# Kernel optimization log

Hardware: AMD Instinct MI355X
Metric: run time of the kernel (lower is better)

The kernel has to match this reference:

```python
import jax, jax.numpy as jnp
import numpy as np


def setup_inputs() -> dict:
    key = jax.random.key(0)
    k1, k2 = jax.random.split(key)
    x = jax.random.normal(k1, (64, 32, 32, 128), dtype=jnp.float32)
    embeddings = jax.random.normal(k2, (128, 1024), dtype=jnp.float32)  # (embedding_dim, num_embeddings)
    return {"x": x, "embeddings": embeddings}


def reference(x, embeddings):
    d = embeddings.shape[0]
    flat = x.reshape(-1, d)  # [N, d]
    # squared L2 distances: ||f||^2 + ||e||^2 - 2 f.e
    similarity = flat @ embeddings  # [N, K]
    distances = (jnp.sum(flat * flat, axis=1, keepdims=True)
                 + jnp.sum(embeddings * embeddings, axis=0)
                 - 2.0 * similarity)
    idx = jnp.argmin(distances, axis=1)  # [N]
    # gather codes (equivalent to one_hot @ embeddings^T)
    quantized = embeddings.T[idx].reshape(x.shape)
    # straight-through estimator
    quantized = x + jax.lax.stop_gradient(quantized - x)
    return quantized
```

## Files before the change

kernel.cpp:

```cpp
#include <hip/hip_runtime.h>


#define NROWS 65536
#define DDIM 128
#define KCODES 1024
#define MARGIN1 0.30f

typedef __attribute__((ext_vector_type(8))) short short8;
typedef __attribute__((ext_vector_type(16))) float f32x16;

__device__ inline ushort f2bf(float f) {
    union { float f; unsigned u; } v; v.f = f;
    unsigned r = v.u + 0x7fffu + ((v.u >> 16) & 1u);
    return (ushort)(r >> 16);
}
__device__ inline float bf2f(ushort b) {
    union { unsigned u; float f; } v; v.u = ((unsigned)b) << 16;
    return v.f;
}

__device__ inline void gload_lds16(const uint4* g, uint4* lds) {
    __builtin_amdgcn_global_load_lds((const __attribute__((address_space(1))) void*)g,
                                     (__attribute__((address_space(3))) void*)lds,
                                     16, 0, 0);
}

__global__ void k_prep(const float* __restrict__ x, const float* __restrict__ e,
                       float* __restrict__ et, float* __restrict__ nrm,
                       double* __restrict__ nrm64, uint4* __restrict__ epq,
                       unsigned* __restrict__ nhl, uint4* __restrict__ xp,
                       int* __restrict__ wlc) {
    const int gid = blockIdx.x * blockDim.x + threadIdx.x;

    if (gid == 0) { wlc[0] = 0; wlc[1] = 0; }

    {
        int lane = gid & 63, c = (gid >> 6) & 7, rt = gid >> 9;
        int row = rt * 32 + (lane & 31);
        int kbase = c * 16 + ((lane >> 5) << 3);
        const float4* xr4 = reinterpret_cast<const float4*>(x + (size_t)row * DDIM + kbase);
        float4 u = xr4[0], v = xr4[1];
        float fv[8] = {u.x, u.y, u.z, u.w, v.x, v.y, v.z, v.w};
        union { ushort s[8]; uint4 q; } pk;
        #pragma unroll
        for (int j = 0; j < 8; ++j) pk.s[j] = f2bf(fv[j]);
        xp[gid] = pk.q;
    }

    if (gid < 131072) {
        int d = gid >> 10, k = gid & 1023;
        et[k * DDIM + d] = e[gid];
    }

    if (gid < 16384) {
        int lane = gid & 63, c = (gid >> 6) & 7, nt = gid >> 9;
        int col = nt * 32 + (lane & 31);
        int kbase = c * 16 + ((lane >> 5) << 3);
        union { ushort s[8]; uint4 q; } pk;
        #pragma unroll
        for (int j = 0; j < 8; ++j)
            pk.s[j] = f2bf(e[(kbase + j) * KCODES + col]);
        epq[(size_t)nt * 512 + c * 64 + lane] = pk.q;
    }

    if (gid >= 32768 && gid < 32768 + 8192) {
        int t2 = gid - 32768;
        int k = t2 >> 3, part = t2 & 7;
        double s = 0.0;
        #pragma unroll
        for (int j = 0; j < 16; ++j) {
            double v = (double)e[(part * 16 + j) * KCODES + k];
            s = fma(v, v, s);
        }
        #pragma unroll
        for (int m = 1; m < 8; m <<= 1) s += __shfl_xor(s, m);
        if (part == 0) {
            nrm64[k] = s; nrm[k] = (float)s;
            float t0 = (float)(-0.5 * s);
            ushort hb = f2bf(t0);
            ushort lb = f2bf(t0 - bf2f(hb));
            nhl[k] = (unsigned)hb | ((unsigned)lb << 16);
        }
    }
}

__global__ __launch_bounds__(256, 3) void k_argmin32(const uint4* __restrict__ xp,
                                                     const uint4* __restrict__ epq,
                                                     const unsigned* __restrict__ nhl,
                                                     unsigned* __restrict__ pb1,
                                                     float* __restrict__ pb2) {
    __shared__ uint4 sbuf[2048];
    __shared__ unsigned snhl[128];

    const int tid = threadIdx.x;
    const int lane = tid & 63;
    const int w = tid >> 6;
    const int kq = blockIdx.x & 7;
    const int rg = blockIdx.x >> 3;
    const int rtA = rg * 8 + w * 2;
    const int rtB = rtA + 1;
    const int lrow = lane & 31;
    const int lgrp = lane >> 5;

    #pragma unroll
    for (int i = 0; i < 8; ++i)
        gload_lds16(epq + (size_t)kq * 2048 + i * 256 + tid,
                    &sbuf[i * 256 + (w << 6)]);
    if (tid < 32)
        gload_lds16(reinterpret_cast<const uint4*>(nhl) + kq * 32 + tid,
                    reinterpret_cast<uint4*>(snhl));

    short8 ahA[8], ahB[8];
    #pragma unroll
    for (int c = 0; c < 8; ++c) {
        union { uint4 q; short8 s; } ua, ub;
        ua.q = xp[(size_t)rtA * 512 + c * 64 + lane];
        ub.q = xp[(size_t)rtB * 512 + c * 64 + lane];
        ahA[c] = ua.s; ahB[c] = ub.s;
    }
    short8 bx = {0, 0, 0, 0, 0, 0, 0, 0};
    if (lgrp == 0) { bx[0] = (short)0x3F80; bx[1] = (short)0x3F80; }

    int cidlow[16];
    #pragma unroll
    for (int r = 0; r < 16; ++r)
        cidlow[r] = (((r & 3) + ((r >> 2) << 3)) | (lgrp << 2));

    asm volatile("s_waitcnt vmcnt(0)" ::: "memory");
    __syncthreads();

    float kA1 = -3.4e38f, kA2 = -3.4e38f;
    float kB1 = -3.4e38f, kB2 = -3.4e38f;

    for (int t = 0; t < 4; ++t) {
        f32x16 aA, aB;
        #pragma unroll
        for (int r = 0; r < 16; ++r) { aA[r] = 0.f; aB[r] = 0.f; }

        #pragma unroll
        for (int c = 0; c < 8; ++c) {
            union { uint4 q; short8 s; } ef;
            ef.q = sbuf[t * 512 + c * 64 + lane];
            aA = __builtin_amdgcn_mfma_f32_32x32x16_bf16(ef.s, ahA[c], aA, 0, 0, 0);
            aB = __builtin_amdgcn_mfma_f32_32x32x16_bf16(ef.s, ahB[c], aB, 0, 0, 0);
        }
        unsigned hl = snhl[t * 32 + lrow];
        short8 ax = {0, 0, 0, 0, 0, 0, 0, 0};
        if (lgrp == 0) { ax[0] = (short)(hl & 0xFFFF); ax[1] = (short)(hl >> 16); }
        aA = __builtin_amdgcn_mfma_f32_32x32x16_bf16(ax, bx, aA, 0, 0, 0);
        aB = __builtin_amdgcn_mfma_f32_32x32x16_bf16(ax, bx, aB, 0, 0, 0);

        #pragma unroll
        for (int r = 0; r < 16; ++r) {
            unsigned cid = (unsigned)((t << 5) | cidlow[r]);
            float keyA = __uint_as_float((__float_as_uint(aA[r]) & 0xFFFFFF00u) | cid);
            float keyB = __uint_as_float((__float_as_uint(aB[r]) & 0xFFFFFF00u) | cid);
            kA2 = fmaxf(kA2, fminf(keyA, kA1));
            kA1 = fmaxf(kA1, keyA);
            kB2 = fmaxf(kB2, fminf(keyB, kB1));
            kB1 = fmaxf(kB1, keyB);
        }
    }

    {
        float o1 = __shfl_xor(kA1, 32);
        float o2 = __shfl_xor(kA2, 32);
        float m1 = fmaxf(kA1, o1);
        float m2 = fmaxf(fmaxf(kA2, o2), fminf(kA1, o1));
        if (lane < 32) {
            size_t o = (size_t)kq * NROWS + rtA * 32 + lrow;
            pb1[o] = __float_as_uint(m1);
            pb2[o] = m2;
        }
    }
    {
        float o1 = __shfl_xor(kB1, 32);
        float o2 = __shfl_xor(kB2, 32);
        float m1 = fmaxf(kB1, o1);
        float m2 = fmaxf(fmaxf(kB2, o2), fminf(kB1, o1));
        if (lane < 32) {
            size_t o = (size_t)kq * NROWS + rtB * 32 + lrow;
            pb1[o] = __float_as_uint(m1);
            pb2[o] = m2;
        }
    }
}

__global__ void k_merge(const unsigned* __restrict__ pb1, const float* __restrict__ pb2,
                        int* __restrict__ idx, int* __restrict__ wlc,
                        int* __restrict__ wl) {
    int r = blockIdx.x * blockDim.x + threadIdx.x;
    float best = -3.4e38f, sec = -3.4e38f; int bq = 0;
    #pragma unroll
    for (int q = 0; q < 8; ++q) {
        float k1 = __uint_as_float(pb1[(size_t)q * NROWS + r]);
        float k2 = pb2[(size_t)q * NROWS + r];
        bool t = k1 > best;
        sec = fmaxf(sec, fmaxf(k2, t ? best : k1));
        bq = t ? q : bq;
        best = t ? k1 : best;
    }
    unsigned ub = __float_as_uint(best);
    int code = bq * 128 + (int)(ub & 255u);
    float m1 = __uint_as_float(ub & 0xFFFFFF00u);
    float m2 = __uint_as_float(__float_as_uint(sec) & 0xFFFFFF00u);
    idx[r] = code;
    if (2.f * (m1 - m2) < MARGIN1) {
        int slot = atomicAdd(wlc, 1);
        wl[slot] = r;
    }
}

__global__ __launch_bounds__(256) void k_rescan(const float* __restrict__ x,
                                                const float* __restrict__ e,
                                                const double* __restrict__ nrm64,
                                                const int* __restrict__ wlc,
                                                const int* __restrict__ wl,
                                                int* __restrict__ idx) {
    __shared__ float  xs[4][DDIM];
    __shared__ double rb1[4][256];
    __shared__ int    ri[4][256];
    const int tid = threadIdx.x, lane = tid & 63, wv = tid >> 6;
    const int n = *wlc;

    for (int i0 = blockIdx.x * 4; i0 < n; i0 += gridDim.x * 4) {
        if (tid < 128) {
            int j = tid >> 5, d4 = tid & 31;
            int ii = i0 + j;
            int row = wl[ii < n ? ii : i0];
            *reinterpret_cast<float4*>(&xs[j][d4 * 4]) =
                *reinterpret_cast<const float4*>(&x[(size_t)row * DDIM + d4 * 4]);
        }
        __syncthreads();

        double acc[4][4];
        #pragma unroll
        for (int kk = 0; kk < 4; ++kk)
            #pragma unroll
            for (int j = 0; j < 4; ++j) acc[kk][j] = 0.0;

        for (int d = 0; d < DDIM; d += 2) {
            double xv0[4], xv1[4];
            #pragma unroll
            for (int j = 0; j < 4; ++j) {
                xv0[j] = (double)xs[j][d];
                xv1[j] = (double)xs[j][d + 1];
            }
            #pragma unroll
            for (int kk = 0; kk < 4; ++kk) {
                double ev0 = (double)e[d * KCODES + kk * 256 + tid];
                double ev1 = (double)e[(d + 1) * KCODES + kk * 256 + tid];
                #pragma unroll
                for (int j = 0; j < 4; ++j) {
                    acc[kk][j] = fma(ev0, xv0[j], acc[kk][j]);
                    acc[kk][j] = fma(ev1, xv1[j], acc[kk][j]);
                }
            }
        }

        #pragma unroll
        for (int j = 0; j < 4; ++j) {
            double b1 = 1e300; int bi = 0;
            #pragma unroll
            for (int kk = 0; kk < 4; ++kk) {
                int k = kk * 256 + tid;
                double s = nrm64[k] - 2.0 * acc[kk][j];
                if (s < b1) { b1 = s; bi = k; }
            }
            rb1[j][tid] = b1; ri[j][tid] = bi;
        }
        __syncthreads();

        {
            double b1 = 1e300; int bi = 0x7FFFFFFF;
            #pragma unroll
            for (int p = 0; p < 4; ++p) {
                int t2 = lane + p * 64;
                double o1 = rb1[wv][t2]; int oi = ri[wv][t2];
                bool take = (o1 < b1) || (o1 == b1 && oi < bi);
                b1 = take ? o1 : b1;
                bi = take ? oi : bi;
            }
            #pragma unroll
            for (int m = 1; m < 64; m <<= 1) {
                double o1 = __shfl_xor(b1, m);
                int    oi = __shfl_xor(bi, m);
                bool take = (o1 < b1) || (o1 == b1 && oi < bi);
                b1 = take ? o1 : b1;
                bi = take ? oi : bi;
            }
            if (lane == 0 && i0 + wv < n)
                idx[wl[i0 + wv]] = bi;
        }
        __syncthreads();
    }
}

__global__ void k_gather(const float* __restrict__ x, const float* __restrict__ et,
                         const int* __restrict__ idxp, float* __restrict__ out) {
    int gid = blockIdx.x * blockDim.x + threadIdx.x;
    int row = gid >> 5, d4 = gid & 31;
    float4 q = reinterpret_cast<const float4*>(et)[(size_t)idxp[row] * 32 + d4];
    float4 xv = reinterpret_cast<const float4*>(x)[gid];
    float4 o;
    o.x = xv.x + (q.x - xv.x);
    o.y = xv.y + (q.y - xv.y);
    o.z = xv.z + (q.z - xv.z);
    o.w = xv.w + (q.w - xv.w);
    reinterpret_cast<float4*>(out)[gid] = o;
}

extern "C" void kernel_launch(void* const* d_in, const int* in_sizes, int n_in,
                              void* d_out, int out_size, void* d_ws, size_t ws_size,
                              hipStream_t stream) {
    const float* x = (const float*)d_in[0];
    const float* e = (const float*)d_in[1];
    float* out = (float*)d_out;

    double*   nrm64 = (double*)d_ws;
    float*    et    = (float*)d_ws + 2048;
    float*    nrm   = et + 131072;
    int*      idx   = (int*)(nrm + 1024);
    int*      wlc   = idx + NROWS;
    int*      wl    = wlc + 4;
    uint4*    epq   = (uint4*)(wl + NROWS);
    unsigned* nhl   = (unsigned*)(epq + 16384);
    unsigned* pb1   = nhl + 1024;
    float*    pb2   = (float*)(pb1 + 8 * NROWS);
    uint4*    xp    = (uint4*)d_out;

    k_prep<<<4096, 256, 0, stream>>>(x, e, et, nrm, nrm64, epq, nhl, xp, wlc);
    k_argmin32<<<2048, 256, 0, stream>>>(xp, epq, nhl, pb1, pb2);
    k_merge<<<NROWS / 256, 256, 0, stream>>>(pb1, pb2, idx, wlc, wl);
    k_rescan<<<1024, 256, 0, stream>>>(x, e, nrm64, wlc, wl, idx);
    k_gather<<<(NROWS * 32) / 256, 256, 0, stream>>>(x, et, idx, out);
}
```

Measured before the change: 95.35 us.

## Tile rescan over 8 rows, transpose partial-best layout, use fmed3 for top-2

The rescan kernel now handles 8 worklist rows per block instead of 4 with half the grid, so each loaded fp64 embedding value feeds twice as many FMAs and global embedding traffic drops. Partial top-2 results are stored row-major (8 per row), which lets the merge kernel read them with two vector loads per array instead of strided scalar loads. The running second-best update uses the fmed3 instruction in place of a min/max pair. The trade-off is a larger accumulator array (32 doubles) in rescan, which raises register pressure, and merge now masks the low bits before comparing.

```diff
diff --git a/kernel.cpp b/kernel.cpp
--- a/kernel.cpp
+++ b/kernel.cpp
@@ -155,9 +155,9 @@
             unsigned cid = (unsigned)((t << 5) | cidlow[r]);
             float keyA = __uint_as_float((__float_as_uint(aA[r]) & 0xFFFFFF00u) | cid);
             float keyB = __uint_as_float((__float_as_uint(aB[r]) & 0xFFFFFF00u) | cid);
-            kA2 = fmaxf(kA2, fminf(keyA, kA1));
+            kA2 = __builtin_amdgcn_fmed3f(kA1, kA2, keyA);
             kA1 = fmaxf(kA1, keyA);
-            kB2 = fmaxf(kB2, fminf(keyB, kB1));
+            kB2 = __builtin_amdgcn_fmed3f(kB1, kB2, keyB);
             kB1 = fmaxf(kB1, keyB);
         }
     }
@@ -165,10 +165,10 @@
     {
         float o1 = __shfl_xor(kA1, 32);
         float o2 = __shfl_xor(kA2, 32);
+        float m2 = __builtin_amdgcn_fmed3f(kA1, o1, fmaxf(kA2, o2));
         float m1 = fmaxf(kA1, o1);
-        float m2 = fmaxf(fmaxf(kA2, o2), fminf(kA1, o1));
         if (lane < 32) {
-            size_t o = (size_t)kq * NROWS + rtA * 32 + lrow;
+            size_t o = (size_t)(rtA * 32 + lrow) * 8 + kq;
             pb1[o] = __float_as_uint(m1);
             pb2[o] = m2;
         }
@@ -176,10 +176,10 @@
     {
         float o1 = __shfl_xor(kB1, 32);
         float o2 = __shfl_xor(kB2, 32);
+        float m2 = __builtin_amdgcn_fmed3f(kB1, o1, fmaxf(kB2, o2));
         float m1 = fmaxf(kB1, o1);
-        float m2 = fmaxf(fmaxf(kB2, o2), fminf(kB1, o1));
         if (lane < 32) {
-            size_t o = (size_t)kq * NROWS + rtB * 32 + lrow;
+            size_t o = (size_t)(rtB * 32 + lrow) * 8 + kq;
             pb1[o] = __float_as_uint(m1);
             pb2[o] = m2;
         }
@@ -190,22 +190,28 @@
                         int* __restrict__ idx, int* __restrict__ wlc,
                         int* __restrict__ wl) {
     int r = blockIdx.x * blockDim.x + threadIdx.x;
-    float best = -3.4e38f, sec = -3.4e38f; int bq = 0;
+    const uint4*  p1 = reinterpret_cast<const uint4*>(pb1 + (size_t)r * 8);
+    const float4* p2 = reinterpret_cast<const float4*>(pb2 + (size_t)r * 8);
+    uint4 A = p1[0], B = p1[1];
+    float4 C = p2[0], D = p2[1];
+    unsigned K[8] = {A.x, A.y, A.z, A.w, B.x, B.y, B.z, B.w};
+    float    S[8] = {C.x, C.y, C.z, C.w, D.x, D.y, D.z, D.w};
+
+    float best = -3.4e38f, sec = -3.4e38f;
+    unsigned ub = 0; int bq = 0;
     #pragma unroll
     for (int q = 0; q < 8; ++q) {
-        float k1 = __uint_as_float(pb1[(size_t)q * NROWS + r]);
-        float k2 = pb2[(size_t)q * NROWS + r];
-        bool t = k1 > best;
-        sec = fmaxf(sec, fmaxf(k2, t ? best : k1));
+        float m  = __uint_as_float(K[q] & 0xFFFFFF00u);
+        float s2 = __uint_as_float(__float_as_uint(S[q]) & 0xFFFFFF00u);
+        bool t = m > best;
+        sec = fmaxf(sec, fmaxf(s2, t ? best : m));
+        ub = t ? K[q] : ub;
         bq = t ? q : bq;
-        best = t ? k1 : best;
-    }
-    unsigned ub = __float_as_uint(best);
+        best = t ? m : best;
+    }
     int code = bq * 128 + (int)(ub & 255u);
-    float m1 = __uint_as_float(ub & 0xFFFFFF00u);
-    float m2 = __uint_as_float(__float_as_uint(sec) & 0xFFFFFF00u);
     idx[r] = code;
-    if (2.f * (m1 - m2) < MARGIN1) {
+    if (2.f * (best - sec) < MARGIN1) {
         int slot = atomicAdd(wlc, 1);
         wl[slot] = r;
     }
@@ -217,14 +223,14 @@
                                                 const int* __restrict__ wlc,
                                                 const int* __restrict__ wl,
                                                 int* __restrict__ idx) {
-    __shared__ float  xs[4][DDIM];
-    __shared__ double rb1[4][256];
-    __shared__ int    ri[4][256];
+    __shared__ float  xs[8][DDIM];
+    __shared__ double rb1[8][256];
+    __shared__ int    ri[8][256];
     const int tid = threadIdx.x, lane = tid & 63, wv = tid >> 6;
     const int n = *wlc;
 
-    for (int i0 = blockIdx.x * 4; i0 < n; i0 += gridDim.x * 4) {
-        if (tid < 128) {
+    for (int i0 = blockIdx.x * 8; i0 < n; i0 += gridDim.x * 8) {
+        {
             int j = tid >> 5, d4 = tid & 31;
             int ii = i0 + j;
             int row = wl[ii < n ? ii : i0];
@@ -233,33 +239,27 @@
         }
         __syncthreads();
 
-        double acc[4][4];
+        double acc[4][8];
         #pragma unroll
         for (int kk = 0; kk < 4; ++kk)
             #pragma unroll
-            for (int j = 0; j < 4; ++j) acc[kk][j] = 0.0;
-
-        for (int d = 0; d < DDIM; d += 2) {
-            double xv0[4], xv1[4];
-            #pragma unroll
-            for (int j = 0; j < 4; ++j) {
-                xv0[j] = (double)xs[j][d];
-                xv1[j] = (double)xs[j][d + 1];
+            for (int j = 0; j < 8; ++j) acc[kk][j] = 0.0;
+
+        for (int d = 0; d < DDIM; ++d) {
+            double xv[8];
+            #pragma unroll
+            for (int j = 0; j < 8; ++j) xv[j] = (double)xs[j][d];
+            #pragma unroll
+            for (int kk = 0; kk < 4; ++kk) {
+                double ev = (double)e[d * KCODES + kk * 256 + tid];
+                #pragma unroll
+                for (int j = 0; j < 8; ++j)
+                    acc[kk][j] = fma(ev, xv[j], acc[kk][j]);
             }
-            #pragma unroll
-            for (int kk = 0; kk < 4; ++kk) {
-                double ev0 = (double)e[d * KCODES + kk * 256 + tid];
-                double ev1 = (double)e[(d + 1) * KCODES + kk * 256 + tid];
-                #pragma unroll
-                for (int j = 0; j < 4; ++j) {
-                    acc[kk][j] = fma(ev0, xv0[j], acc[kk][j]);
-                    acc[kk][j] = fma(ev1, xv1[j], acc[kk][j]);
-                }
-            }
-        }
-
-        #pragma unroll
-        for (int j = 0; j < 4; ++j) {
+        }
+
+        #pragma unroll
+        for (int j = 0; j < 8; ++j) {
             double b1 = 1e300; int bi = 0;
             #pragma unroll
             for (int kk = 0; kk < 4; ++kk) {
@@ -271,12 +271,14 @@
         }
         __syncthreads();
 
-        {
+        #pragma unroll
+        for (int jj = 0; jj < 2; ++jj) {
+            int j = wv + jj * 4;
             double b1 = 1e300; int bi = 0x7FFFFFFF;
             #pragma unroll
             for (int p = 0; p < 4; ++p) {
                 int t2 = lane + p * 64;
-                double o1 = rb1[wv][t2]; int oi = ri[wv][t2];
+                double o1 = rb1[j][t2]; int oi = ri[j][t2];
                 bool take = (o1 < b1) || (o1 == b1 && oi < bi);
                 b1 = take ? o1 : b1;
                 bi = take ? oi : bi;
@@ -289,8 +291,8 @@
                 b1 = take ? o1 : b1;
                 bi = take ? oi : bi;
             }
-            if (lane == 0 && i0 + wv < n)
-                idx[wl[i0 + wv]] = bi;
+            if (lane == 0 && i0 + j < n)
+                idx[wl[i0 + j]] = bi;
         }
         __syncthreads();
     }
@@ -332,6 +334,6 @@
     k_prep<<<4096, 256, 0, stream>>>(x, e, et, nrm, nrm64, epq, nhl, xp, wlc);
     k_argmin32<<<2048, 256, 0, stream>>>(xp, epq, nhl, pb1, pb2);
     k_merge<<<NROWS / 256, 256, 0, stream>>>(pb1, pb2, idx, wlc, wl);
-    k_rescan<<<1024, 256, 0, stream>>>(x, e, nrm64, wlc, wl, idx);
+    k_rescan<<<512, 256, 0, stream>>>(x, e, nrm64, wlc, wl, idx);
     k_gather<<<(NROWS * 32) / 256, 256, 0, stream>>>(x, et, idx, out);
 }
```

Result: slower. 226.5 us (+137.5%).
